# Kernel tuning notes

Hardware: AMD Instinct MI355X
Metric: run time of the kernel (lower is better)

Reference implementation:

```python
import jax, jax.numpy as jnp
import numpy as np

MIN_HALF_LIFE = 15.0 / (24 * 60)   # days
MAX_HALF_LIFE = 274.0              # days
SECONDS_PER_DAY = 60.0 * 60.0 * 24.0
BASE = 2.0

B, N, T = 256, 512, 200


def setup_inputs() -> dict:
    key = jax.random.key(0)
    k0, k1, k2, k3, k4 = jax.random.split(key, 5)
    x0 = jax.random.uniform(k0, (B, N), dtype=jnp.float32)
    # sorted timestamps in seconds: cumulative gaps of up to ~2 days
    gaps = jax.random.uniform(k1, (B, T), dtype=jnp.float32, minval=60.0, maxval=2.0 * SECONDS_PER_DAY)
    t = jnp.cumsum(gaps, axis=-1)
    items = jax.random.randint(k2, (B, T), 0, N, dtype=jnp.int64)
    # history stats [N_total, N_success, N_failure], small non-negative counts
    stats = jax.random.randint(k3, (B, N, T, 3), 0, 20).astype(jnp.float32)
    theta = jax.random.normal(k4, (3,), dtype=jnp.float32) * 0.05  # xavier-ish scale for (1,3)
    return {"x0": x0, "t": t, "items": items, "stats": stats, "theta": theta}


def reference(x0, t, items, stats, theta):
    # train mode, stats precomputed -> loop over timesteps vectorizes exactly.
    feats = stats[:, :, :-1, :]                      # [B, N, T-1, 3] (step i uses stats at i-1)
    # half_life = hclip(base ** (feat @ theta))
    logits = jnp.einsum('bntk,k->bnt', feats, theta)  # [B, N, T-1]
    half_life = jnp.clip(jnp.exp2(logits), MIN_HALF_LIFE, MAX_HALF_LIFE)
    dt = jnp.diff(t, axis=-1)[:, None, :] / SECONDS_PER_DAY  # [B, 1, T-1] days (tiled over nodes)
    p_all = jax.nn.sigmoid(jnp.exp2(-dt / half_life))        # [B, N, T-1]
    # x_pred = [x0, p_all_1, ..., p_all_{T-1}] stacked on last axis -> [B, N, T]
    x_pred = jnp.concatenate([x0[..., None], p_all], axis=-1)
    # p_item: gather p_all at items[:, i] for i = 1..T-1
    idx = items[:, None, 1:]                                 # [B, 1, T-1]
    x_item_pred = jnp.take_along_axis(p_all, idx, axis=1)[:, 0, :]  # [B, T-1]
    return x_pred, x_item_pred, half_life
```

## Files before the change

kernel.cpp:

```cpp
#include <hip/hip_runtime.h>

constexpr int B = 256, N = 512, T = 200, TM1 = 199;
constexpr int SLOTS = (TM1 + 3) / 4;
constexpr float MIN_HL = 15.0f / (24.0f * 60.0f);
constexpr float MAX_HL = 274.0f;
constexpr float INV_SPD = 1.0f / 86400.0f;

__device__ __forceinline__ float hl_of(float s0, float s1, float s2,
                                       float th0, float th1, float th2) {
    float logit = fmaf(s0, th0, fmaf(s1, th1, s2 * th2));
    return fminf(fmaxf(exp2f(logit), MIN_HL), MAX_HL);
}

__device__ __forceinline__ float p_of(float hl, float dt_days) {
    float z = exp2f(-dt_days / hl);
    return 1.0f / (1.0f + __expf(-z));
}

__global__ __launch_bounds__(256) void hlr_main(
    const float* __restrict__ x0,
    const float* __restrict__ t,
    const float* __restrict__ stats,
    const float* __restrict__ theta,
    float* __restrict__ x_pred,
    float* __restrict__ half_life)
{
    const unsigned idx = blockIdx.x * 256u + threadIdx.x;
    const unsigned row = idx / SLOTS;
    if (row >= (unsigned)(B * N)) return;
    const unsigned slot = idx - row * SLOTS;
    const unsigned b = row >> 9;
    const int j0 = slot * 4;

    const float th0 = theta[0], th1 = theta[1], th2 = theta[2];

    const float4* sp = reinterpret_cast<const float4*>(
        stats + (size_t)row * (T * 3) + (size_t)j0 * 3);
    const float4 sA = sp[0];
    const float4 sB = sp[1];
    const float4 sC = sp[2];

    const float* trow = t + (size_t)b * T;
    const float t0 = trow[j0];
    const float t1 = trow[j0 + 1];
    const float t2 = trow[j0 + 2];
    const float t3 = trow[j0 + 3];
    const float t4 = (j0 + 4 < T) ? trow[j0 + 4] : 0.f;

    const float hl0 = hl_of(sA.x, sA.y, sA.z, th0, th1, th2);
    const float hl1 = hl_of(sA.w, sB.x, sB.y, th0, th1, th2);
    const float hl2 = hl_of(sB.z, sB.w, sC.x, th0, th1, th2);
    const float hl3 = hl_of(sC.y, sC.z, sC.w, th0, th1, th2);

    const float p0 = p_of(hl0, (t1 - t0) * INV_SPD);
    const float p1 = p_of(hl1, (t2 - t1) * INV_SPD);
    const float p2 = p_of(hl2, (t3 - t2) * INV_SPD);
    const float p3 = p_of(hl3, (t4 - t3) * INV_SPD);

    float* xp = x_pred + (size_t)row * T;
    float* hp = half_life + (size_t)row * TM1;

    if (slot == 0) xp[0] = x0[row];

    xp[j0 + 1] = p0;  hp[j0]     = hl0;
    xp[j0 + 2] = p1;  hp[j0 + 1] = hl1;
    xp[j0 + 3] = p2;  hp[j0 + 2] = hl2;
    if (j0 + 3 < TM1) { xp[j0 + 4] = p3; hp[j0 + 3] = hl3; }
}

__global__ __launch_bounds__(256) void hlr_item(
    const float* __restrict__ t,
    const int* __restrict__ items,
    const float* __restrict__ stats,
    const float* __restrict__ theta,
    float* __restrict__ x_item)
{
    const int i = blockIdx.x * 256 + threadIdx.x;
    if (i >= B * TM1) return;
    const int b = i / TM1;
    const int j = i - b * TM1;
    const int n = items[(size_t)b * T + j + 1];

    const float th0 = theta[0], th1 = theta[1], th2 = theta[2];
    const float* s = stats + ((size_t)(b * N + n) * T + j) * 3;
    const float hl = hl_of(s[0], s[1], s[2], th0, th1, th2);
    const float dt = (t[(size_t)b * T + j + 1] - t[(size_t)b * T + j]) * INV_SPD;
    x_item[i] = p_of(hl, dt);
}

extern "C" void kernel_launch(void* const* d_in, const int* in_sizes, int n_in,
                              void* d_out, int out_size, void* d_ws, size_t ws_size,
                              hipStream_t stream) {
    const float* x0    = (const float*)d_in[0];
    const float* t     = (const float*)d_in[1];
    const int*   items = (const int*)d_in[2];
    const float* stats = (const float*)d_in[3];
    const float* theta = (const float*)d_in[4];

    float* out = (float*)d_out;
    float* x_pred    = out;
    float* x_item    = out + (size_t)B * N * T;
    float* half_life = out + (size_t)B * N * T + (size_t)B * TM1;

    {
        const unsigned total = (unsigned)(B * N) * SLOTS;
        const unsigned blocks = (total + 255) / 256;
        hlr_main<<<blocks, 256, 0, stream>>>(x0, t, stats, theta, x_pred, half_life);
    }
    {
        const int total = B * TM1;
        const int blocks = (total + 255) / 256;
        hlr_item<<<blocks, 256, 0, stream>>>(t, items, stats, theta, x_item);
    }
}
```

Before: 102.5 us.

## Fuse main and item kernels, widen per-thread work to 8 steps, nontemporal memory ops

```diff
diff --git a/kernel.cpp b/kernel.cpp
--- a/kernel.cpp
+++ b/kernel.cpp
@@ -1,7 +1,13 @@
 #include <hip/hip_runtime.h>
 
+typedef float f32x4 __attribute__((ext_vector_type(4)));
+
 constexpr int B = 256, N = 512, T = 200, TM1 = 199;
-constexpr int SLOTS = (TM1 + 3) / 4;
+constexpr int JPT = 8;
+constexpr int SLOTS = 25;
+constexpr unsigned MAIN_THREADS = (unsigned)B * N * SLOTS;
+constexpr unsigned MAIN_BLOCKS  = MAIN_THREADS / 256;
+constexpr unsigned ITEM_BLOCKS  = ((unsigned)B * TM1) / 256;
 constexpr float MIN_HL = 15.0f / (24.0f * 60.0f);
 constexpr float MAX_HL = 274.0f;
 constexpr float INV_SPD = 1.0f / 86400.0f;
@@ -17,75 +23,75 @@
     return 1.0f / (1.0f + __expf(-z));
 }
 
-__global__ __launch_bounds__(256) void hlr_main(
+__global__ __launch_bounds__(256) void hlr_fused(
     const float* __restrict__ x0,
     const float* __restrict__ t,
+    const int*   __restrict__ items,
     const float* __restrict__ stats,
     const float* __restrict__ theta,
     float* __restrict__ x_pred,
+    float* __restrict__ x_item,
     float* __restrict__ half_life)
 {
-    const unsigned idx = blockIdx.x * 256u + threadIdx.x;
-    const unsigned row = idx / SLOTS;
-    if (row >= (unsigned)(B * N)) return;
-    const unsigned slot = idx - row * SLOTS;
-    const unsigned b = row >> 9;
-    const int j0 = slot * 4;
+    const float th0 = theta[0], th1 = theta[1], th2 = theta[2];
+    const unsigned bid = blockIdx.x;
 
-    const float th0 = theta[0], th1 = theta[1], th2 = theta[2];
+    if (bid < MAIN_BLOCKS) {
+        const unsigned idx  = bid * 256u + threadIdx.x;
+        const unsigned row  = idx / SLOTS;
+        const unsigned slot = idx - row * SLOTS;
+        const unsigned b    = row >> 9;
+        const int j0 = slot * JPT;
 
-    const float4* sp = reinterpret_cast<const float4*>(
-        stats + (size_t)row * (T * 3) + (size_t)j0 * 3);
-    const float4 sA = sp[0];
-    const float4 sB = sp[1];
-    const float4 sC = sp[2];
+        const f32x4* sp = reinterpret_cast<const f32x4*>(
+            stats + (size_t)row * (T * 3) + (size_t)j0 * 3);
+        float s[24];
+        f32x4* sv = reinterpret_cast<f32x4*>(s);
+        #pragma unroll
+        for (int k = 0; k < 6; ++k) sv[k] = __builtin_nontemporal_load(sp + k);
 
-    const float* trow = t + (size_t)b * T;
-    const float t0 = trow[j0];
-    const float t1 = trow[j0 + 1];
-    const float t2 = trow[j0 + 2];
-    const float t3 = trow[j0 + 3];
-    const float t4 = (j0 + 4 < T) ? trow[j0 + 4] : 0.f;
+        const float* trow = t + (size_t)b * T;
+        const f32x4 ta = *reinterpret_cast<const f32x4*>(trow + j0);
+        const f32x4 tb = *reinterpret_cast<const f32x4*>(trow + j0 + 4);
+        const float t8 = (j0 + 8 < T) ? trow[j0 + 8] : 0.f;
+        const float tt[9] = {ta.x, ta.y, ta.z, ta.w, tb.x, tb.y, tb.z, tb.w, t8};
 
-    const float hl0 = hl_of(sA.x, sA.y, sA.z, th0, th1, th2);
-    const float hl1 = hl_of(sA.w, sB.x, sB.y, th0, th1, th2);
-    const float hl2 = hl_of(sB.z, sB.w, sC.x, th0, th1, th2);
-    const float hl3 = hl_of(sC.y, sC.z, sC.w, th0, th1, th2);
+        float hl[JPT], p[JPT];
+        #pragma unroll
+        for (int i = 0; i < JPT; ++i) {
+            hl[i] = hl_of(s[3*i], s[3*i+1], s[3*i+2], th0, th1, th2);
+            p[i]  = p_of(hl[i], (tt[i+1] - tt[i]) * INV_SPD);
+        }
 
-    const float p0 = p_of(hl0, (t1 - t0) * INV_SPD);
-    const float p1 = p_of(hl1, (t2 - t1) * INV_SPD);
-    const float p2 = p_of(hl2, (t3 - t2) * INV_SPD);
-    const float p3 = p_of(hl3, (t4 - t3) * INV_SPD);
+        float* xp = x_pred    + (size_t)row * T;
+        float* hp = half_life + (size_t)row * TM1;
 
-    float* xp = x_pred + (size_t)row * T;
-    float* hp = half_life + (size_t)row * TM1;
+        if (slot == 0) __builtin_nontemporal_store(x0[row], xp);
 
-    if (slot == 0) xp[0] = x0[row];
+        if (slot != SLOTS - 1) {
+            #pragma unroll
+            for (int i = 0; i < JPT; ++i) {
+                __builtin_nontemporal_store(p[i],  xp + j0 + 1 + i);
+                __builtin_nontemporal_store(hl[i], hp + j0 + i);
+            }
+        } else {
+            #pragma unroll
+            for (int i = 0; i < JPT - 1; ++i) {
+                __builtin_nontemporal_store(p[i],  xp + j0 + 1 + i);
+                __builtin_nontemporal_store(hl[i], hp + j0 + i);
+            }
+        }
+    } else {
+        const int i = (int)(bid - MAIN_BLOCKS) * 256 + (int)threadIdx.x;
+        const int b = i / TM1;
+        const int j = i - b * TM1;
+        const int n = items[(size_t)b * T + j + 1];
 
-    xp[j0 + 1] = p0;  hp[j0]     = hl0;
-    xp[j0 + 2] = p1;  hp[j0 + 1] = hl1;
-    xp[j0 + 3] = p2;  hp[j0 + 2] = hl2;
-    if (j0 + 3 < TM1) { xp[j0 + 4] = p3; hp[j0 + 3] = hl3; }
-}
-
-__global__ __launch_bounds__(256) void hlr_item(
-    const float* __restrict__ t,
-    const int* __restrict__ items,
-    const float* __restrict__ stats,
-    const float* __restrict__ theta,
-    float* __restrict__ x_item)
-{
-    const int i = blockIdx.x * 256 + threadIdx.x;
-    if (i >= B * TM1) return;
-    const int b = i / TM1;
-    const int j = i - b * TM1;
-    const int n = items[(size_t)b * T + j + 1];
-
-    const float th0 = theta[0], th1 = theta[1], th2 = theta[2];
-    const float* s = stats + ((size_t)(b * N + n) * T + j) * 3;
-    const float hl = hl_of(s[0], s[1], s[2], th0, th1, th2);
-    const float dt = (t[(size_t)b * T + j + 1] - t[(size_t)b * T + j]) * INV_SPD;
-    x_item[i] = p_of(hl, dt);
+        const float* sg = stats + ((size_t)((size_t)b * N + n) * T + j) * 3;
+        const float hl = hl_of(sg[0], sg[1], sg[2], th0, th1, th2);
+        const float dt = (t[(size_t)b * T + j + 1] - t[(size_t)b * T + j]) * INV_SPD;
+        __builtin_nontemporal_store(p_of(hl, dt), x_item + i);
+    }
 }
 
 extern "C" void kernel_launch(void* const* d_in, const int* in_sizes, int n_in,
@@ -102,14 +108,6 @@
     float* x_item    = out + (size_t)B * N * T;
     float* half_life = out + (size_t)B * N * T + (size_t)B * TM1;
 
-    {
-        const unsigned total = (unsigned)(B * N) * SLOTS;
-        const unsigned blocks = (total + 255) / 256;
-        hlr_main<<<blocks, 256, 0, stream>>>(x0, t, stats, theta, x_pred, half_life);
-    }
-    {
-        const int total = B * TM1;
-        const int blocks = (total + 255) / 256;
-        hlr_item<<<blocks, 256, 0, stream>>>(t, items, stats, theta, x_item);
-    }
+    hlr_fused<<<MAIN_BLOCKS + ITEM_BLOCKS, 256, 0, stream>>>(
+        x0, t, items, stats, theta, x_pred, x_item, half_life);
 }
```

Result: slower. 183.7 us (+79.3%).
